# Kernel tuning notes

Hardware: AMD Instinct MI355X
Metric: run time of the kernel (lower is better)

## Reference

```python
import jax, jax.numpy as jnp
from jax import lax
import numpy as np

EPS = 1e-5
DN = ('NCHW', 'OIHW', 'NCHW')
# Sum of the four Sobel-like kernels used in sobel_conv2d (conv is linear, so
# summing four depthwise convs == one depthwise conv with the summed kernel).
SOBEL_SUM = jnp.array([[2., 4., 4.], [-2., 0., 2.], [-4., -4., -2.]], dtype=jnp.float32)


def conv_bn_relu(x, w, b, g, be, m, v, pad):
    y = lax.conv_general_dilated(x, w, (1, 1), [(pad, pad), (pad, pad)], dimension_numbers=DN)
    y = y + b[None, :, None, None]
    inv = g * lax.rsqrt(v + EPS)
    y = (y - m[None, :, None, None]) * inv[None, :, None, None] + be[None, :, None, None]
    return jax.nn.relu(y)


def sobel_depthwise(x):
    C = x.shape[1]
    k = jnp.broadcast_to(SOBEL_SUM[None, None], (C, 1, 3, 3))
    return lax.conv_general_dilated(x, k, (1, 1), [(1, 1), (1, 1)],
                                    dimension_numbers=DN, feature_group_count=C)


def setup_inputs() -> dict:
    key = jax.random.key(0)
    ks = jax.random.split(key, 20)
    B, Cin, H, W = 16, 64, 128, 128
    Co = 256  # out_channels
    d = {'input_f': jax.random.normal(ks[0], (B, Cin, H, W), jnp.float32)}

    def bn(i, c):
        return (jax.random.normal(ks[i], (c,), jnp.float32) * 0.1 + 1.0,  # gamma
                jax.random.normal(ks[i + 1], (c,), jnp.float32) * 0.1,    # beta
                jax.random.normal(ks[i + 2], (c,), jnp.float32) * 0.1,    # running mean
                jax.random.uniform(ks[i + 3], (c,), jnp.float32, 0.5, 1.5))  # running var

    d['w1'] = jax.random.normal(ks[1], (Co, Cin, 1, 1), jnp.float32) * (1.0 / np.sqrt(Cin))
    d['b1'] = jnp.zeros((Co,), jnp.float32)
    d['g1'], d['be1'], d['m1'], d['v1'] = bn(2, Co)
    d['w2'] = jax.random.normal(ks[6], (Co // 2, Co, 3, 3), jnp.float32) * (1.0 / np.sqrt(Co * 9))
    d['b2'] = jnp.zeros((Co // 2,), jnp.float32)
    d['g2'], d['be2'], d['m2'], d['v2'] = bn(7, Co // 2)
    d['w3'] = jax.random.normal(ks[11], (Co // 4, Co // 2, 3, 3), jnp.float32) * (1.0 / np.sqrt(Co // 2 * 9))
    d['b3'] = jnp.zeros((Co // 4,), jnp.float32)
    d['g3'], d['be3'], d['m3'], d['v3'] = bn(12, Co // 4)
    return d


def reference(input_f, w1, b1, g1, be1, m1, v1, w2, b2, g2, be2, m2, v2,
              w3, b3, g3, be3, m3, v3):
    c1 = conv_bn_relu(input_f, w1, b1, g1, be1, m1, v1, pad=0)  # [B,256,H,W]
    c2 = conv_bn_relu(c1, w2, b2, g2, be2, m2, v2, pad=1)       # [B,128,H,W]
    edge = sobel_depthwise(c2)                                   # [B,128,H,W]
    c3 = conv_bn_relu(edge, w3, b3, g3, be3, m3, v3, pad=1)     # [B,64,H,W]
    return jnp.concatenate([input_f, c3], axis=1)                # [B,128,H,W]
```

## Files before the change

kernel.cpp:

```cpp
#include <hip/hip_runtime.h>

#define HW 16384
#define EPSF 1e-5f

typedef __attribute__((ext_vector_type(8))) short s8v;
typedef __attribute__((ext_vector_type(16))) float f16v;

__device__ __forceinline__ ushort f2b(float f) {
    union { float f; unsigned u; } v; v.f = f;
    return (ushort)((v.u + 0x7FFFu + ((v.u >> 16) & 1u)) >> 16);
}
__device__ __forceinline__ float b2f(ushort h) {
    union { unsigned u; float f; } v; v.u = ((unsigned)h) << 16; return v.f;
}


__global__ void bn_prep(const float* __restrict__ b1, const float* __restrict__ g1,
                        const float* __restrict__ be1, const float* __restrict__ m1,
                        const float* __restrict__ v1,
                        const float* __restrict__ b2, const float* __restrict__ g2,
                        const float* __restrict__ be2, const float* __restrict__ m2,
                        const float* __restrict__ v2,
                        const float* __restrict__ b3, const float* __restrict__ g3,
                        const float* __restrict__ be3, const float* __restrict__ m3,
                        const float* __restrict__ v3,
                        float* __restrict__ ws) {
    int t = threadIdx.x;
    if (t < 256) { float a = g1[t] * rsqrtf(v1[t] + EPSF); ws[t] = a;       ws[256 + t] = (b1[t] - m1[t]) * a + be1[t]; }
    if (t < 128) { float a = g2[t] * rsqrtf(v2[t] + EPSF); ws[512 + t] = a; ws[640 + t] = (b2[t] - m2[t]) * a + be2[t]; }
    if (t < 64)  { float a = g3[t] * rsqrtf(v3[t] + EPSF); ws[768 + t] = a; ws[832 + t] = (b3[t] - m3[t]) * a + be3[t]; }
}

__global__ __launch_bounds__(256) void wprep(const float* __restrict__ w2, const float* __restrict__ w3,
                                             const float* __restrict__ w1,
                                             ushort* __restrict__ w2b, ushort* __restrict__ w3b,
                                             ushort* __restrict__ w1b) {
    int t = blockIdx.x * 256 + threadIdx.x;
    if (t < 9 * 128 * 256) {
        int off = t >> 15; int r = t & 32767; int co = r >> 8; int ci = r & 255;
        w2b[t] = f2b(w2[(co * 256 + ci) * 9 + off]);
    }
    t -= 9 * 128 * 256;
    if (t >= 0 && t < 9 * 64 * 128) {
        int off = t >> 13; int r = t & 8191; int co = r >> 7; int ci = r & 127;
        w3b[t] = f2b(w3[(co * 128 + ci) * 9 + off]);
    }
    t -= 9 * 64 * 128;
    if (t >= 0 && t < 256 * 64) {
        w1b[t] = f2b(w1[t]);
    }
}

__global__ __launch_bounds__(256) void copy_in_k(const float* __restrict__ x, float* __restrict__ out) {
    size_t i = (size_t)blockIdx.x * 256 + threadIdx.x;
    size_t b = i >> 18;
    size_t r = i & 262143;
    ((float4*)out)[b * (size_t)(128 * HW / 4) + r] = ((const float4*)x)[i];
}

__global__ __launch_bounds__(256, 2)
void conv1_mfma(const float* __restrict__ x, const ushort* __restrict__ w1b,
                const float* __restrict__ alpha, const float* __restrict__ beta,
                ushort* __restrict__ c1u, int b0) {
    __shared__ __align__(16) ushort sW[256][72];
    const int tid = threadIdx.x;
    const int lane = tid & 63;
    const int wid = tid >> 6;
    const int l31 = lane & 31;
    const int l5 = lane >> 5;
    const int bz = blockIdx.x >> 7;
    const int y  = blockIdx.x & 127;
    const int px = wid * 32 + l31;

#pragma unroll
    for (int it = 0; it < 8; ++it) {
        const int idx = it * 256 + tid;
        const int co = idx >> 3, cig = idx & 7;
        *(int4*)&sW[co][cig * 8] = *(const int4*)&w1b[co * 64 + cig * 8];
    }

    const float* xp = x + ((size_t)(b0 + bz) * 64 + l5 * 8) * HW + y * 128 + px;
    float xv[32];
#pragma unroll
    for (int s = 0; s < 4; ++s)
#pragma unroll
        for (int j = 0; j < 8; ++j)
            xv[s * 8 + j] = xp[(size_t)(s * 16 + j) * HW];

    union { ushort u[8]; s8v v; } hf[4], lf[4];
#pragma unroll
    for (int s = 0; s < 4; ++s)
#pragma unroll
        for (int j = 0; j < 8; ++j) {
            union { float f; unsigned u; } t0; t0.f = xv[s * 8 + j];
            hf[s].u[j] = (ushort)(t0.u >> 16);
            union { unsigned u; float f; } t1; t1.u = t0.u & 0xFFFF0000u;
            lf[s].u[j] = f2b(t0.f - t1.f);
        }

    f16v acc[8];
#pragma unroll
    for (int ct = 0; ct < 8; ++ct) acc[ct] = (f16v)(0.0f);

    __syncthreads();
#pragma unroll
    for (int s = 0; s < 4; ++s) {
#pragma unroll
        for (int ct = 0; ct < 8; ++ct) {
            const s8v af = *(const s8v*)&sW[ct * 32 + l31][s * 16 + l5 * 8];
            acc[ct] = __builtin_amdgcn_mfma_f32_32x32x16_bf16(af, hf[s].v, acc[ct], 0, 0, 0);
            acc[ct] = __builtin_amdgcn_mfma_f32_32x32x16_bf16(af, lf[s].v, acc[ct], 0, 0, 0);
        }
    }

    ushort* sT = &sW[0][0];
    const int piece = y >> 6;
    const size_t base = (size_t)(2 * bz + piece) * 4194304 + (size_t)(y & 63) * 128 * 256;
#pragma unroll
    for (int p = 0; p < 2; ++p) {
        __syncthreads();
#pragma unroll
        for (int c4 = 0; c4 < 4; ++c4) {
            const int ct = p * 4 + c4;
#pragma unroll
            for (int rg = 0; rg < 4; ++rg) {
                const int co = c4 * 32 + rg * 8 + l5 * 4;
                const float4 av = *(const float4*)&alpha[p * 128 + co];
                const float4 bv = *(const float4*)&beta[p * 128 + co];
                ushort4 o;
                o.x = f2b(fmaxf(acc[ct][rg * 4 + 0] * av.x + bv.x, 0.f));
                o.y = f2b(fmaxf(acc[ct][rg * 4 + 1] * av.y + bv.y, 0.f));
                o.z = f2b(fmaxf(acc[ct][rg * 4 + 2] * av.z + bv.z, 0.f));
                o.w = f2b(fmaxf(acc[ct][rg * 4 + 3] * av.w + bv.w, 0.f));
                *(ushort4*)&sT[px * 136 + co] = o;
            }
        }
        __syncthreads();
#pragma unroll
        for (int it = 0; it < 8; ++it) {
            const int idx = it * 256 + tid;
            const int pxx = idx >> 4, c16 = idx & 15;
            const int4 v = *(const int4*)&sT[pxx * 136 + c16 * 8];
            *(int4*)&c1u[base + (size_t)pxx * 256 + p * 128 + c16 * 8] = v;
        }
    }
}

__global__ __launch_bounds__(256, 2)
void conv2_mfma(const ushort* __restrict__ c1u, const ushort* __restrict__ wb,
                const float* __restrict__ alpha, const float* __restrict__ beta,
                ushort* __restrict__ ybf, int b0) {
    constexpr int CI = 256, CO = 128, MT = 2;
    __shared__ __align__(16) ushort sX[2][130][40];
    __shared__ __align__(16) ushort sW[3][CO][40];
    const int tid = threadIdx.x;
    const int lane = tid & 63;
    const int wid = tid >> 6;
    const int wm = wid & 1;
    const int wr = wid >> 1;
    const int l31 = lane & 31;
    const int l5 = lane >> 5;
    const int bz = blockIdx.x >> 6;
    const int y0 = (blockIdx.x & 63) * 2;

    f16v acc[MT][4];
#pragma unroll
    for (int mt = 0; mt < MT; ++mt)
#pragma unroll
        for (int nt = 0; nt < 4; ++nt) acc[mt][nt] = (f16v)(0.0f);

    if (tid < 128) {
        int r = tid >> 6, rem = tid & 63;
        int p = (rem < 32) ? 0 : 129;
        sX[r][p][rem & 31] = 0;
    }

    for (int dy = 0; dy < 3; ++dy) {
        for (int cc = 0; cc < CI; cc += 32) {
            __syncthreads();
#pragma unroll
            for (int it = 0; it < 4; ++it) {
                const int idx = it * 256 + tid;
                const int r = idx >> 9, xx = (idx >> 2) & 127, cig = idx & 3;
                const int yy = y0 + r + dy - 1;
                int4 v = make_int4(0, 0, 0, 0);
                if ((unsigned)yy < 128u) {
                    const size_t base = (size_t)(2 * bz + (yy >> 6)) * 4194304;
                    v = *(const int4*)&c1u[base + (((yy & 63) * 128 + xx) * 256 + cc + cig * 8)];
                }
                *(int4*)&sX[r][xx + 1][cig * 8] = v;
            }
#pragma unroll
            for (int it = 0; it < 6; ++it) {
                const int idx = it * 256 + tid;
                const int dxs = idx >> 9;
                const int r = idx & 511;
                const int co = r >> 2, cig = r & 3;
                *(int4*)&sW[dxs][co][cig * 8] =
                    *(const int4*)&wb[((size_t)((dy * 3 + dxs) * CO) + co) * CI + cc + cig * 8];
            }
            __syncthreads();
#pragma unroll
            for (int dx = 0; dx < 3; ++dx) {
#pragma unroll
                for (int kh = 0; kh < 2; ++kh) {
                    s8v af[MT], bfr[4];
#pragma unroll
                    for (int mt = 0; mt < MT; ++mt)
                        af[mt] = *(const s8v*)&sW[dx][wm * 64 + mt * 32 + l31][kh * 16 + l5 * 8];
#pragma unroll
                    for (int nt = 0; nt < 4; ++nt)
                        bfr[nt] = *(const s8v*)&sX[wr][nt * 32 + l31 + dx][kh * 16 + l5 * 8];
#pragma unroll
                    for (int mt = 0; mt < MT; ++mt)
#pragma unroll
                        for (int nt = 0; nt < 4; ++nt)
                            acc[mt][nt] = __builtin_amdgcn_mfma_f32_32x32x16_bf16(
                                af[mt], bfr[nt], acc[mt][nt], 0, 0, 0);
                }
            }
        }
    }
    const int yy = y0 + wr;
    const size_t cb2 = (size_t)(b0 + bz) * 4194304 + 2097152;
#pragma unroll
    for (int mt = 0; mt < MT; ++mt) {
#pragma unroll
        for (int nt = 0; nt < 4; ++nt) {
            const int xx = nt * 32 + l31;
#pragma unroll
            for (int rg = 0; rg < 4; ++rg) {
                const int co0 = wm * 64 + mt * 32 + rg * 8 + l5 * 4;
                const float4 av = *(const float4*)&alpha[co0];
                const float4 bv = *(const float4*)&beta[co0];
                ushort4 o;
                o.x = f2b(fmaxf(acc[mt][nt][rg * 4 + 0] * av.x + bv.x, 0.f));
                o.y = f2b(fmaxf(acc[mt][nt][rg * 4 + 1] * av.y + bv.y, 0.f));
                o.z = f2b(fmaxf(acc[mt][nt][rg * 4 + 2] * av.z + bv.z, 0.f));
                o.w = f2b(fmaxf(acc[mt][nt][rg * 4 + 3] * av.w + bv.w, 0.f));
                *(ushort4*)&ybf[cb2 + ((size_t)yy * 128 + xx) * 128 + co0] = o;
            }
        }
    }
}

__global__ __launch_bounds__(256)
void sobel_nhwc(const ushort* __restrict__ outu, ushort* __restrict__ edgeu) {
    const int tid = threadIdx.x;
    const int cg = tid & 15;
    const int xl = tid >> 4;
    const int xblk = blockIdx.x & 7;
    const int y = (blockIdx.x >> 3) & 127;
    const int b = blockIdx.x >> 10;
    const int x = xblk * 16 + xl;
    const size_t cb2 = (size_t)b * 4194304 + 2097152;
    const size_t eb = (size_t)b * 4194304;
    float acc[8];
#pragma unroll
    for (int j = 0; j < 8; ++j) acc[j] = 0.f;
    const float cf[9] = {2.f, 4.f, 4.f, -2.f, 0.f, 2.f, -4.f, -4.f, -2.f};
#pragma unroll
    for (int t = 0; t < 9; ++t) {
        if (t == 4) continue;
        const int yy = y + (t / 3) - 1, xx = x + (t % 3) - 1;
        if ((unsigned)yy < 128u && (unsigned)xx < 128u) {
            union { int4 v; ushort s[8]; } u;
            u.v = *(const int4*)&outu[cb2 + ((size_t)yy * 128 + xx) * 128 + cg * 8];
            const float c = cf[t];
#pragma unroll
            for (int j = 0; j < 8; ++j) acc[j] += c * b2f(u.s[j]);
        }
    }
    union { ushort s[8]; int4 v; } o;
#pragma unroll
    for (int j = 0; j < 8; ++j) o.s[j] = f2b(acc[j]);
    *(int4*)&edgeu[eb + ((size_t)y * 128 + x) * 128 + cg * 8] = o.v;
}

__global__ __launch_bounds__(256, 2)
void conv3_mfma(const ushort* __restrict__ edgeu, const ushort* __restrict__ wb,
                const float* __restrict__ alpha, const float* __restrict__ beta,
                float* __restrict__ out) {
    constexpr int CI = 128, CO = 64;
    __shared__ __align__(16) ushort sX[2][130][72];
    __shared__ __align__(16) ushort sW[3][CO][72];
    const int tid = threadIdx.x;
    const int lane = tid & 63;
    const int wid = tid >> 6;
    const int wm = wid & 1;
    const int wr = wid >> 1;
    const int l31 = lane & 31;
    const int l5 = lane >> 5;
    const int b = blockIdx.x >> 6;
    const int y0 = (blockIdx.x & 63) * 2;
    const size_t eb = (size_t)b * 4194304;

    f16v acc[4];
#pragma unroll
    for (int nt = 0; nt < 4; ++nt) acc[nt] = (f16v)(0.0f);

    {
        int r = tid >> 7, rem = tid & 127;
        int p = (rem < 64) ? 0 : 129;
        sX[r][p][rem & 63] = 0;
    }

    for (int dy = 0; dy < 3; ++dy) {
        for (int cc = 0; cc < CI; cc += 64) {
            __syncthreads();
#pragma unroll
            for (int it = 0; it < 8; ++it) {
                const int idx = it * 256 + tid;
                const int r = idx >> 10, xx = (idx >> 3) & 127, cig = idx & 7;
                const int yy = y0 + r + dy - 1;
                int4 v = make_int4(0, 0, 0, 0);
                if ((unsigned)yy < 128u)
                    v = *(const int4*)&edgeu[eb + ((size_t)yy * 128 + xx) * CI + cc + cig * 8];
                *(int4*)&sX[r][xx + 1][cig * 8] = v;
            }
#pragma unroll
            for (int it = 0; it < 6; ++it) {
                const int idx = it * 256 + tid;
                const int dxs = idx >> 9;
                const int r = idx & 511;
                const int co = r >> 3, cig = r & 7;
                *(int4*)&sW[dxs][co][cig * 8] =
                    *(const int4*)&wb[((size_t)((dy * 3 + dxs) * CO) + co) * CI + cc + cig * 8];
            }
            __syncthreads();
#pragma unroll
            for (int dx = 0; dx < 3; ++dx) {
#pragma unroll
                for (int kh = 0; kh < 4; ++kh) {
                    const s8v af = *(const s8v*)&sW[dx][wm * 32 + l31][kh * 16 + l5 * 8];
                    s8v bfr[4];
#pragma unroll
                    for (int nt = 0; nt < 4; ++nt)
                        bfr[nt] = *(const s8v*)&sX[wr][nt * 32 + l31 + dx][kh * 16 + l5 * 8];
#pragma unroll
                    for (int nt = 0; nt < 4; ++nt)
                        acc[nt] = __builtin_amdgcn_mfma_f32_32x32x16_bf16(af, bfr[nt], acc[nt], 0, 0, 0);
                }
            }
        }
    }
    const int yy = y0 + wr;
#pragma unroll
    for (int nt = 0; nt < 4; ++nt) {
        const int xx = nt * 32 + l31;
#pragma unroll
        for (int rg = 0; rg < 4; ++rg) {
            const int co0 = wm * 32 + rg * 8 + l5 * 4;
            const float4 av = *(const float4*)&alpha[co0];
            const float4 bv = *(const float4*)&beta[co0];
            const size_t base = ((size_t)b * 128 + 64 + co0) * HW + yy * 128 + xx;
            out[base]          = fmaxf(acc[nt][rg * 4 + 0] * av.x + bv.x, 0.f);
            out[base + HW]     = fmaxf(acc[nt][rg * 4 + 1] * av.y + bv.y, 0.f);
            out[base + 2 * HW] = fmaxf(acc[nt][rg * 4 + 2] * av.z + bv.z, 0.f);
            out[base + 3 * HW] = fmaxf(acc[nt][rg * 4 + 3] * av.w + bv.w, 0.f);
        }
    }
}

extern "C" void kernel_launch(void* const* d_in, const int* in_sizes, int n_in,
                              void* d_out, int out_size, void* d_ws, size_t ws_size,
                              hipStream_t stream) {
    const float* input = (const float*)d_in[0];
    const float* w1 = (const float*)d_in[1];
    const float* b1 = (const float*)d_in[2];
    const float* g1 = (const float*)d_in[3];
    const float* be1 = (const float*)d_in[4];
    const float* m1 = (const float*)d_in[5];
    const float* v1 = (const float*)d_in[6];
    const float* w2 = (const float*)d_in[7];
    const float* b2 = (const float*)d_in[8];
    const float* g2 = (const float*)d_in[9];
    const float* be2 = (const float*)d_in[10];
    const float* m2 = (const float*)d_in[11];
    const float* v2 = (const float*)d_in[12];
    const float* w3 = (const float*)d_in[13];
    const float* b3 = (const float*)d_in[14];
    const float* g3 = (const float*)d_in[15];
    const float* be3 = (const float*)d_in[16];
    const float* m3 = (const float*)d_in[17];
    const float* v3 = (const float*)d_in[18];
    float* ws = (float*)d_ws;
    float* out = (float*)d_out;
    ushort* outu = (ushort*)d_out;

    float* A1 = ws;        float* B1 = ws + 256;
    float* A2 = ws + 512;  float* B2 = ws + 640;
    float* A3 = ws + 768;  float* B3 = ws + 832;

    char* wsb = (char*)d_ws;
    ushort* w1b = (ushort*)(wsb + 4096);
    ushort* w2b = (ushort*)(wsb + 4096 + 32768);
    ushort* w3b = (ushort*)(wsb + 4096 + 32768 + 589824);

    bn_prep<<<1, 256, 0, stream>>>(b1, g1, be1, m1, v1, b2, g2, be2, m2, v2,
                                   b3, g3, be3, m3, v3, ws);
    wprep<<<1505, 256, 0, stream>>>(w2, w3, w1, w2b, w3b, w1b);

    for (int b0 = 0; b0 < 16; b0 += 8) {
        conv1_mfma<<<1024, 256, 0, stream>>>(input, w1b, A1, B1, outu, b0);
        conv2_mfma<<<512, 256, 0, stream>>>(outu, w2b, A2, B2, outu, b0);
    }
    sobel_nhwc<<<16384, 256, 0, stream>>>(outu, outu);
    conv3_mfma<<<1024, 256, 0, stream>>>(outu, w3b, A3, B3, out);
    copy_in_k<<<16384, 256, 0, stream>>>(input, out);
}
```

Before: 499.4 us.

## Stage 4-row halo tile once per channel chunk to reuse inputs across dy

Both 3x3 conv kernels now load a 4-row input tile (2 output rows plus halo) and all 9 filter taps for a 16-channel chunk, then loop over dy and dx inside. Previously each dy iteration reloaded the input rows from global memory, so every input row was fetched three times. The intent is to cut global and LDS load traffic for the input tile. In exchange, the channel chunk shrinks to 16 (conv2 was 32, conv3 was 64), so there are more chunk iterations and barriers, and each chunk does less MFMA work to hide load latency.

```diff
diff --git a/kernel.cpp b/kernel.cpp
--- a/kernel.cpp
+++ b/kernel.cpp
@@ -151,8 +151,8 @@
                 const float* __restrict__ alpha, const float* __restrict__ beta,
                 ushort* __restrict__ ybf, int b0) {
     constexpr int CI = 256, CO = 128, MT = 2;
-    __shared__ __align__(16) ushort sX[2][130][40];
-    __shared__ __align__(16) ushort sW[3][CO][40];
+    __shared__ __align__(16) ushort sX[4][130][24];
+    __shared__ __align__(16) ushort sW[9][CO][16];
     const int tid = threadIdx.x;
     const int lane = tid & 63;
     const int wid = tid >> 6;
@@ -170,54 +170,51 @@
         for (int nt = 0; nt < 4; ++nt) acc[mt][nt] = (f16v)(0.0f);
 
     if (tid < 128) {
-        int r = tid >> 6, rem = tid & 63;
-        int p = (rem < 32) ? 0 : 129;
-        sX[r][p][rem & 31] = 0;
-    }
-
-    for (int dy = 0; dy < 3; ++dy) {
-        for (int cc = 0; cc < CI; cc += 32) {
-            __syncthreads();
-#pragma unroll
-            for (int it = 0; it < 4; ++it) {
-                const int idx = it * 256 + tid;
-                const int r = idx >> 9, xx = (idx >> 2) & 127, cig = idx & 3;
-                const int yy = y0 + r + dy - 1;
-                int4 v = make_int4(0, 0, 0, 0);
-                if ((unsigned)yy < 128u) {
-                    const size_t base = (size_t)(2 * bz + (yy >> 6)) * 4194304;
-                    v = *(const int4*)&c1u[base + (((yy & 63) * 128 + xx) * 256 + cc + cig * 8)];
-                }
-                *(int4*)&sX[r][xx + 1][cig * 8] = v;
-            }
-#pragma unroll
-            for (int it = 0; it < 6; ++it) {
-                const int idx = it * 256 + tid;
-                const int dxs = idx >> 9;
-                const int r = idx & 511;
-                const int co = r >> 2, cig = r & 3;
-                *(int4*)&sW[dxs][co][cig * 8] =
-                    *(const int4*)&wb[((size_t)((dy * 3 + dxs) * CO) + co) * CI + cc + cig * 8];
-            }
-            __syncthreads();
+        int r = tid >> 5, rem = tid & 31;
+        int p = (rem < 16) ? 0 : 129;
+        sX[r][p][rem & 15] = 0;
+    }
+
+    for (int cc = 0; cc < CI; cc += 16) {
+        __syncthreads();
+#pragma unroll
+        for (int it = 0; it < 4; ++it) {
+            const int idx = it * 256 + tid;
+            const int r = idx >> 8, xx = (idx >> 1) & 127, cig = idx & 1;
+            const int yy = y0 + r - 1;
+            int4 v = make_int4(0, 0, 0, 0);
+            if ((unsigned)yy < 128u) {
+                const size_t base = (size_t)(2 * bz + (yy >> 6)) * 4194304;
+                v = *(const int4*)&c1u[base + (((yy & 63) * 128 + xx) * 256 + cc + cig * 8)];
+            }
+            *(int4*)&sX[r][xx + 1][cig * 8] = v;
+        }
+#pragma unroll
+        for (int it = 0; it < 9; ++it) {
+            const int idx = it * 256 + tid;
+            const int off = idx >> 8, co = (idx >> 1) & 127, cig = idx & 1;
+            *(int4*)&sW[off][co][cig * 8] =
+                *(const int4*)&wb[((size_t)(off * CO) + co) * CI + cc + cig * 8];
+        }
+        __syncthreads();
+#pragma unroll
+        for (int dy = 0; dy < 3; ++dy) {
 #pragma unroll
             for (int dx = 0; dx < 3; ++dx) {
-#pragma unroll
-                for (int kh = 0; kh < 2; ++kh) {
-                    s8v af[MT], bfr[4];
-#pragma unroll
-                    for (int mt = 0; mt < MT; ++mt)
-                        af[mt] = *(const s8v*)&sW[dx][wm * 64 + mt * 32 + l31][kh * 16 + l5 * 8];
+                const int off = dy * 3 + dx;
+                s8v af[MT], bfr[4];
+#pragma unroll
+                for (int mt = 0; mt < MT; ++mt)
+                    af[mt] = *(const s8v*)&sW[off][wm * 64 + mt * 32 + l31][l5 * 8];
+#pragma unroll
+                for (int nt = 0; nt < 4; ++nt)
+                    bfr[nt] = *(const s8v*)&sX[wr + dy][nt * 32 + l31 + dx][l5 * 8];
+#pragma unroll
+                for (int mt = 0; mt < MT; ++mt)
 #pragma unroll
                     for (int nt = 0; nt < 4; ++nt)
-                        bfr[nt] = *(const s8v*)&sX[wr][nt * 32 + l31 + dx][kh * 16 + l5 * 8];
-#pragma unroll
-                    for (int mt = 0; mt < MT; ++mt)
-#pragma unroll
-                        for (int nt = 0; nt < 4; ++nt)
-                            acc[mt][nt] = __builtin_amdgcn_mfma_f32_32x32x16_bf16(
-                                af[mt], bfr[nt], acc[mt][nt], 0, 0, 0);
-                }
+                        acc[mt][nt] = __builtin_amdgcn_mfma_f32_32x32x16_bf16(
+                            af[mt], bfr[nt], acc[mt][nt], 0, 0, 0);
             }
         }
     }
@@ -282,8 +279,8 @@
                 const float* __restrict__ alpha, const float* __restrict__ beta,
                 float* __restrict__ out) {
     constexpr int CI = 128, CO = 64;
-    __shared__ __align__(16) ushort sX[2][130][72];
-    __shared__ __align__(16) ushort sW[3][CO][72];
+    __shared__ __align__(16) ushort sX[4][130][24];
+    __shared__ __align__(16) ushort sW[9][CO][16];
     const int tid = threadIdx.x;
     const int lane = tid & 63;
     const int wid = tid >> 6;
@@ -299,48 +296,47 @@
 #pragma unroll
     for (int nt = 0; nt < 4; ++nt) acc[nt] = (f16v)(0.0f);
 
-    {
-        int r = tid >> 7, rem = tid & 127;
-        int p = (rem < 64) ? 0 : 129;
-        sX[r][p][rem & 63] = 0;
-    }
-
-    for (int dy = 0; dy < 3; ++dy) {
-        for (int cc = 0; cc < CI; cc += 64) {
-            __syncthreads();
-#pragma unroll
-            for (int it = 0; it < 8; ++it) {
-                const int idx = it * 256 + tid;
-                const int r = idx >> 10, xx = (idx >> 3) & 127, cig = idx & 7;
-                const int yy = y0 + r + dy - 1;
-                int4 v = make_int4(0, 0, 0, 0);
-                if ((unsigned)yy < 128u)
-                    v = *(const int4*)&edgeu[eb + ((size_t)yy * 128 + xx) * CI + cc + cig * 8];
-                *(int4*)&sX[r][xx + 1][cig * 8] = v;
-            }
-#pragma unroll
-            for (int it = 0; it < 6; ++it) {
-                const int idx = it * 256 + tid;
-                const int dxs = idx >> 9;
-                const int r = idx & 511;
-                const int co = r >> 3, cig = r & 7;
-                *(int4*)&sW[dxs][co][cig * 8] =
-                    *(const int4*)&wb[((size_t)((dy * 3 + dxs) * CO) + co) * CI + cc + cig * 8];
-            }
-            __syncthreads();
+    if (tid < 128) {
+        int r = tid >> 5, rem = tid & 31;
+        int p = (rem < 16) ? 0 : 129;
+        sX[r][p][rem & 15] = 0;
+    }
+
+    for (int cc = 0; cc < CI; cc += 16) {
+        __syncthreads();
+#pragma unroll
+        for (int it = 0; it < 4; ++it) {
+            const int idx = it * 256 + tid;
+            const int r = idx >> 8, xx = (idx >> 1) & 127, cig = idx & 1;
+            const int yy = y0 + r - 1;
+            int4 v = make_int4(0, 0, 0, 0);
+            if ((unsigned)yy < 128u)
+                v = *(const int4*)&edgeu[eb + ((size_t)yy * 128 + xx) * CI + cc + cig * 8];
+            *(int4*)&sX[r][xx + 1][cig * 8] = v;
+        }
+#pragma unroll
+        for (int it = 0; it < 5; ++it) {
+            const int idx = it * 256 + tid;
+            if (idx < 1152) {
+                const int off = idx >> 7, co = (idx >> 1) & 63, cig = idx & 1;
+                *(int4*)&sW[off][co][cig * 8] =
+                    *(const int4*)&wb[((size_t)(off * CO) + co) * CI + cc + cig * 8];
+            }
+        }
+        __syncthreads();
+#pragma unroll
+        for (int dy = 0; dy < 3; ++dy) {
 #pragma unroll
             for (int dx = 0; dx < 3; ++dx) {
-#pragma unroll
-                for (int kh = 0; kh < 4; ++kh) {
-                    const s8v af = *(const s8v*)&sW[dx][wm * 32 + l31][kh * 16 + l5 * 8];
-                    s8v bfr[4];
-#pragma unroll
-                    for (int nt = 0; nt < 4; ++nt)
-                        bfr[nt] = *(const s8v*)&sX[wr][nt * 32 + l31 + dx][kh * 16 + l5 * 8];
-#pragma unroll
-                    for (int nt = 0; nt < 4; ++nt)
-                        acc[nt] = __builtin_amdgcn_mfma_f32_32x32x16_bf16(af, bfr[nt], acc[nt], 0, 0, 0);
-                }
+                const int off = dy * 3 + dx;
+                const s8v af = *(const s8v*)&sW[off][wm * 32 + l31][l5 * 8];
+                s8v bfr[4];
+#pragma unroll
+                for (int nt = 0; nt < 4; ++nt)
+                    bfr[nt] = *(const s8v*)&sX[wr + dy][nt * 32 + l31 + dx][l5 * 8];
+#pragma unroll
+                for (int nt = 0; nt < 4; ++nt)
+                    acc[nt] = __builtin_amdgcn_mfma_f32_32x32x16_bf16(af, bfr[nt], acc[nt], 0, 0, 0);
             }
         }
     }
```

New measurement: 577.0 us. 1.16x slower.
